# Performance work log

Hardware: AMD Instinct MI355X
Metric: run time of the kernel (lower is better)

## Reference

```python
import jax, jax.numpy as jnp
import numpy as np
from jax import lax

S, T, B, I, H = 10, 256, 128, 128, 128


def setup_inputs() -> dict:
    key = jax.random.key(0)
    ks = jax.random.split(key, 32)
    stdv = 1.0 / np.sqrt(H)
    u = lambda k, shp: jax.random.uniform(k, shp, jnp.float32, -stdv, stdv)
    inp = {
        'features': jax.random.normal(ks[0], (S, T, B, I), jnp.float32),
        # 10 parallel cuDNN-style LSTMs (PyTorch gate order i,f,g,o)
        'lstm_Wih': u(ks[1], (S, 4 * H, I)),
        'lstm_Whh': u(ks[2], (S, 4 * H, H)),
        'lstm_bih': u(ks[3], (S, 4 * H)),
        'lstm_bhh': u(ks[4], (S, 4 * H)),
        # MI-LSTM: per-stream input gate + candidate, shared f/o gates, attention Wa
        'mi_Wi': u(ks[5], (S, H, H)), 'mi_Ui': u(ks[6], (S, H, H)), 'mi_bi': u(ks[7], (S, H)),
        'mi_Wc': u(ks[8], (S, H, H)), 'mi_Uc': u(ks[9], (S, H, H)), 'mi_bc': u(ks[10], (S, H)),
        'mi_Wf': u(ks[11], (H, H)), 'mi_Uf': u(ks[12], (H, H)), 'mi_bf': u(ks[13], (H,)),
        'mi_Wo': u(ks[14], (H, H)), 'mi_Uo': u(ks[15], (H, H)), 'mi_bo': u(ks[16], (H,)),
        'mi_Wa': u(ks[17], (H, H)),
        'head_W': u(ks[18], (H, 1)), 'head_b': u(ks[19], (1,)),
    }
    return inp


def _lstm(x, Wih, Whh, bih, bhh):
    # x: [T,B,I]; returns hidden sequence [T,B,H]
    gx = jnp.einsum('tbi,gi->tbg', x, Wih) + bih + bhh  # [T,B,4H]

    def step(carry, gx_t):
        h, c = carry
        g = gx_t + h @ Whh.T
        i, f, gg, o = jnp.split(g, 4, axis=-1)
        c = jax.nn.sigmoid(f) * c + jax.nn.sigmoid(i) * jnp.tanh(gg)
        h = jax.nn.sigmoid(o) * jnp.tanh(c)
        return (h, c), h

    z = jnp.zeros((x.shape[1], Whh.shape[1]), x.dtype)
    _, hs = lax.scan(step, (z, z), gx)
    return hs


def _forward(features, lstm_Wih, lstm_Whh, lstm_bih, lstm_bhh,
             mi_Wi, mi_Ui, mi_bi, mi_Wc, mi_Uc, mi_bc,
             mi_Wf, mi_Uf, mi_bf, mi_Wo, mi_Uo, mi_bo,
             mi_Wa, head_W, head_b):
    # 10 parallel LSTM streams, relu'd outputs -> [S,T,B,H]
    tilde = jax.nn.relu(jax.vmap(_lstm)(features, lstm_Wih, lstm_Whh, lstm_bih, lstm_bhh))

    # precompute input-side gate projections (time-parallel)
    xi = jnp.einsum('ktbh,khd->tkbd', tilde, mi_Wi) + mi_bi[:, None, :]   # [T,S,B,H]
    xc = jnp.einsum('ktbh,khd->tkbd', tilde, mi_Wc) + mi_bc[:, None, :]
    y = tilde[0]                                                          # mainstream [T,B,H]
    xf = y @ mi_Wf + mi_bf                                                # [T,B,H]
    xo = y @ mi_Wo + mi_bo

    def step(carry, xs):
        h, c = carry
        xi_t, xc_t, xf_t, xo_t = xs
        i = jax.nn.sigmoid(xi_t + jnp.einsum('bh,khd->kbd', h, mi_Ui))    # [S,B,H]
        ctil = jnp.tanh(xc_t + jnp.einsum('bh,khd->kbd', h, mi_Uc))
        l = i * ctil                                                      # per-stream cell update
        # attention over the S streams, keyed on previous cell state
        u = jnp.tanh(jnp.einsum('kbh,bh->kb', l, c @ mi_Wa))              # [S,B]
        alpha = jax.nn.softmax(u, axis=0)
        lmix = jnp.einsum('kb,kbh->bh', alpha, l)                         # [B,H]
        f = jax.nn.sigmoid(xf_t + h @ mi_Uf)
        o = jax.nn.sigmoid(xo_t + h @ mi_Uo)
        c_new = f * c + lmix
        h_new = o * jnp.tanh(c_new)
        return (h_new, c_new), h_new

    z = jnp.zeros((B, H), features.dtype)
    _, hs = lax.scan(step, (z, z), (xi, xc, xf, xo))                      # hs: [T,B,H]

    out = jax.nn.relu(jax.nn.relu(hs) @ head_W + head_b)                  # [T,B,1]
    return out


def reference(features, lstm_Wih, lstm_Whh, lstm_bih, lstm_bhh,
              mi_Wi, mi_Ui, mi_bi, mi_Wc, mi_Uc, mi_bc,
              mi_Wf, mi_Uf, mi_bf, mi_Wo, mi_Uo, mi_bo,
              mi_Wa, head_W, head_b):
    return _forward(features, lstm_Wih, lstm_Whh, lstm_bih, lstm_bhh,
                    mi_Wi, mi_Ui, mi_bi, mi_Wc, mi_Uc, mi_bc,
                    mi_Wf, mi_Uf, mi_bf, mi_Wo, mi_Uo, mi_bo,
                    mi_Wa, head_W, head_b)
```

## Files before the change

kernel.cpp:

```cpp
#include <hip/hip_runtime.h>
#include <math.h>

#define SS 10
#define TT 256
#define BB 128
#define HH 128
#define II 128
#define G4 512
#define ZK 256
#define NCOL 2944
#define NBLK 184

#define SZ_W2T   (SS*ZK*G4)
#define SZ_BIAS2 (SS*G4)
#define SZ_UBIG  (HH*NCOL)
#define SZ_TILDE (SS*TT*BB*HH)
#define SZ_X     (TT*SS*BB*HH)
#define SZ_XFO   (TT*BB*HH)

#define OFF_W2T   0
#define OFF_BIAS2 (OFF_W2T + SZ_W2T)
#define OFF_UBIG  (OFF_BIAS2 + SZ_BIAS2)
#define OFF_TILDE (OFF_UBIG + SZ_UBIG)
#define OFF_XI    (OFF_TILDE + SZ_TILDE)
#define OFF_XC    (OFF_XI + SZ_X)
#define OFF_XF    (OFF_XC + SZ_X)
#define OFF_XO    (OFF_XF + SZ_XFO)
#define OFF_HT    (OFF_XO + SZ_XFO)
#define OFF_CT    (OFF_HT + BB*HH)
#define OFF_ACT   (OFF_CT + BB*HH)
#define OFF_CNT   (OFF_ACT + BB*NCOL)

__device__ __forceinline__ float sigf(float x){ return 1.0f/(1.0f+expf(-x)); }

__device__ __forceinline__ float ald(const float* p){
  return __hip_atomic_load(p, __ATOMIC_RELAXED, __HIP_MEMORY_SCOPE_AGENT);
}
__device__ __forceinline__ void ast(float* p, float v){
  __hip_atomic_store(p, v, __ATOMIC_RELAXED, __HIP_MEMORY_SCOPE_AGENT);
}
__device__ __forceinline__ int aldi(const int* p){
  return __hip_atomic_load(p, __ATOMIC_RELAXED, __HIP_MEMORY_SCOPE_AGENT);
}
__device__ __forceinline__ void asti(int* p, int v){
  __hip_atomic_store(p, v, __ATOMIC_RELAXED, __HIP_MEMORY_SCOPE_AGENT);
}
typedef float f32x4v __attribute__((ext_vector_type(4)));
__device__ __forceinline__ void ast4(float* p, float a, float b, float c, float d){
  f32x4v w; w.x = a; w.y = b; w.z = c; w.w = d;
  asm volatile("global_store_dwordx4 %0, %1, off sc0 sc1" :: "v"(p), "v"(w) : "memory");
}
__device__ __forceinline__ f32x4v ald4(const float* p){
  f32x4v r;
  asm volatile("global_load_dwordx4 %0, %1, off sc0 sc1" : "=v"(r) : "v"(p) : "memory");
  return r;
}

__global__ __launch_bounds__(256) void prep_w2t(const float* __restrict__ Wih, const float* __restrict__ Whh,
                                                const float* __restrict__ bih, const float* __restrict__ bhh,
                                                float* __restrict__ w2t, float* __restrict__ bias2){
  int idx = blockIdx.x*256 + threadIdx.x;
  if (idx < SZ_W2T){
    int q = idx & 3; int j = (idx >> 2) & 511; int kk4 = (idx >> 11) & 63; int s = idx >> 17;
    int kk = kk4*4 + q;
    float v = (kk < II) ? Wih[(s*G4 + j)*II + kk] : Whh[(s*G4 + j)*HH + (kk - II)];
    w2t[idx] = v;
  }
  if (idx < SZ_BIAS2) bias2[idx] = bih[idx] + bhh[idx];
}

__global__ __launch_bounds__(256) void prep_ubig(const float* __restrict__ Ui, const float* __restrict__ Uc,
                                                 const float* __restrict__ Uf, const float* __restrict__ Uo,
                                                 const float* __restrict__ Wa, float* __restrict__ ubig){
  int idx = blockIdx.x*256 + threadIdx.x;
  if (idx >= SZ_UBIG) return;
  int col = idx % NCOL; int h = idx / NCOL;
  float v;
  if (col < 1280){ int k = col >> 7, d = col & 127; v = Ui[(k*HH + h)*HH + d]; }
  else if (col < 2560){ int c2 = col - 1280; int k = c2 >> 7, d = c2 & 127; v = Uc[(k*HH + h)*HH + d]; }
  else if (col < 2688){ v = Uf[h*HH + (col - 2560)]; }
  else if (col < 2816){ v = Uo[h*HH + (col - 2688)]; }
  else               { v = Wa[h*HH + (col - 2816)]; }
  ubig[idx] = v;
}

__global__ __launch_bounds__(256) void init_state(int* flags, float* hR, float* cR){
  int idx = blockIdx.x*256 + threadIdx.x;
  if (idx < 384) flags[idx] = 0;
  if (idx < BB*HH){ hR[idx] = 0.f; cR[idx] = 0.f; }
}

__global__ __launch_bounds__(1024) void lstm_scan(const float* __restrict__ feat, const float* __restrict__ w2t,
                                                  const float* __restrict__ bias2, float* __restrict__ tilde){
  int p = blockIdx.x;
  int g = (p & 7) * 20 + (p >> 3);
  int s = g >> 4; int rb = g & 15; int b0 = rb * 8;
  const int tid = threadIdx.x;
  const int j = tid & 511;
  const int half = tid >> 9;
  __shared__ float z[8][ZK];
  __shared__ float glp[8][G4];
  __shared__ float gl[8][G4];
  const float* w2ts = w2t + (size_t)s*ZK*G4;
  const float* wb = w2ts + ((size_t)(half*32)*G4 + j)*4;
  float bj = (half == 0) ? bias2[s*G4 + j] : 0.f;
  const int r8 = tid >> 7;
  const int k8 = tid & 127;
  float c = 0.f;
  z[r8][128 + k8] = 0.f;
  z[r8][k8] = feat[((s*TT + 0)*BB + (b0 + r8))*II + k8];
  __syncthreads();
  for (int t = 0; t < TT; ++t){
    float acc[8];
    #pragma unroll
    for (int r=0;r<8;++r) acc[r] = bj;
    const float* wp = wb;
    const int kb0 = half*128;
    for (int kk4 = 0; kk4 < 32; ++kk4){
      float4 wv = *(const float4*)wp;
      wp += 4*G4;
      #pragma unroll
      for (int r=0;r<8;++r){
        float4 zv = *(const float4*)&z[r][kb0 + kk4*4];
        acc[r] = fmaf(zv.w, wv.w, fmaf(zv.z, wv.z, fmaf(zv.y, wv.y, fmaf(zv.x, wv.x, acc[r]))));
      }
    }
    if (half == 1){
      #pragma unroll
      for (int r=0;r<8;++r) glp[r][j] = acc[r];
    }
    __syncthreads();
    if (half == 0){
      int gtype = j >> 7;
      #pragma unroll
      for (int r=0;r<8;++r){
        float v = acc[r] + glp[r][j];
        v = (gtype == 2) ? tanhf(v) : sigf(v);
        gl[r][j] = v;
      }
    }
    __syncthreads();
    {
      float si = gl[r8][k8];
      float sf = gl[r8][128 + k8];
      float tg = gl[r8][256 + k8];
      float so = gl[r8][384 + k8];
      c = sf*c + si*tg;
      float h = so*tanhf(c);
      z[r8][128 + k8] = h;
      tilde[((s*TT + t)*BB + (b0 + r8))*HH + k8] = fmaxf(h, 0.f);
      if (t+1 < TT)
        z[r8][k8] = feat[((s*TT + (t+1))*BB + (b0 + r8))*II + k8];
    }
    __syncthreads();
  }
}

__global__ __launch_bounds__(256) void proj_ic(const float* __restrict__ tilde,
                                               const float* __restrict__ Wi, const float* __restrict__ bi,
                                               const float* __restrict__ Wc, const float* __restrict__ bc,
                                               float* __restrict__ xi, float* __restrict__ xc){
  const int k = blockIdx.y;
  const int isc = blockIdx.z;
  const float* W = (isc ? Wc : Wi) + k*HH*HH;
  const float* bias = (isc ? bc : bi) + k*HH;
  float* out = isc ? xc : xi;
  const int m0 = blockIdx.x * 128;
  const int tid = threadIdx.x;
  __shared__ float Wl[HH*HH];
  __shared__ float Al[32*HH];
  for (int u = 0; u < 64; ++u) Wl[u*256 + tid] = W[u*256 + tid];
  const int tx = tid & 31, ty = tid >> 5;
  const int d0 = tx*4;
  float4 bv = *(const float4*)&bias[d0];
  __syncthreads();
  for (int ch = 0; ch < 4; ++ch){
    const float* Arow = tilde + (size_t)(k*TT*BB + m0 + ch*32)*HH;
    #pragma unroll
    for (int u = 0; u < 4; ++u)
      *(float4*)&Al[u*1024 + tid*4] = *(const float4*)&Arow[u*1024 + tid*4];
    __syncthreads();
    float4 a0 = bv, a1 = bv, a2 = bv, a3 = bv;
    for (int h = 0; h < HH; ++h){
      float4 w4 = *(const float4*)&Wl[h*HH + d0];
      float A0 = Al[(ty   )*HH + h], A1 = Al[(ty+ 8)*HH + h];
      float A2 = Al[(ty+16)*HH + h], A3 = Al[(ty+24)*HH + h];
      a0.x = fmaf(A0,w4.x,a0.x); a0.y = fmaf(A0,w4.y,a0.y); a0.z = fmaf(A0,w4.z,a0.z); a0.w = fmaf(A0,w4.w,a0.w);
      a1.x = fmaf(A1,w4.x,a1.x); a1.y = fmaf(A1,w4.y,a1.y); a1.z = fmaf(A1,w4.z,a1.z); a1.w = fmaf(A1,w4.w,a1.w);
      a2.x = fmaf(A2,w4.x,a2.x); a2.y = fmaf(A2,w4.y,a2.y); a2.z = fmaf(A2,w4.z,a2.z); a2.w = fmaf(A2,w4.w,a2.w);
      a3.x = fmaf(A3,w4.x,a3.x); a3.y = fmaf(A3,w4.y,a3.y); a3.z = fmaf(A3,w4.z,a3.z); a3.w = fmaf(A3,w4.w,a3.w);
    }
    float4 accs[4] = {a0,a1,a2,a3};
    #pragma unroll
    for (int i = 0; i < 4; ++i){
      int m = m0 + ch*32 + ty + 8*i;
      int t = m >> 7, b = m & 127;
      *(float4*)&out[((t*SS + k)*BB + b)*HH + d0] = accs[i];
    }
    __syncthreads();
  }
}

__global__ __launch_bounds__(256) void proj_fo(const float* __restrict__ tilde,
                                               const float* __restrict__ Wf, const float* __restrict__ bf,
                                               const float* __restrict__ Wo, const float* __restrict__ bo,
                                               float* __restrict__ xf, float* __restrict__ xo){
  const int iso = blockIdx.y;
  const float* W = iso ? Wo : Wf;
  const float* bias = iso ? bo : bf;
  float* out = iso ? xo : xf;
  const int m0 = blockIdx.x * 128;
  const int tid = threadIdx.x;
  __shared__ float Wl[HH*HH];
  __shared__ float Al[32*HH];
  for (int u = 0; u < 64; ++u) Wl[u*256 + tid] = W[u*256 + tid];
  const int tx = tid & 31, ty = tid >> 5;
  const int d0 = tx*4;
  float4 bv = *(const float4*)&bias[d0];
  __syncthreads();
  for (int ch = 0; ch < 4; ++ch){
    const float* Arow = tilde + (size_t)(m0 + ch*32)*HH;
    #pragma unroll
    for (int u = 0; u < 4; ++u)
      *(float4*)&Al[u*1024 + tid*4] = *(const float4*)&Arow[u*1024 + tid*4];
    __syncthreads();
    float4 a0 = bv, a1 = bv, a2 = bv, a3 = bv;
    for (int h = 0; h < HH; ++h){
      float4 w4 = *(const float4*)&Wl[h*HH + d0];
      float A0 = Al[(ty   )*HH + h], A1 = Al[(ty+ 8)*HH + h];
      float A2 = Al[(ty+16)*HH + h], A3 = Al[(ty+24)*HH + h];
      a0.x = fmaf(A0,w4.x,a0.x); a0.y = fmaf(A0,w4.y,a0.y); a0.z = fmaf(A0,w4.z,a0.z); a0.w = fmaf(A0,w4.w,a0.w);
      a1.x = fmaf(A1,w4.x,a1.x); a1.y = fmaf(A1,w4.y,a1.y); a1.z = fmaf(A1,w4.z,a1.z); a1.w = fmaf(A1,w4.w,a1.w);
      a2.x = fmaf(A2,w4.x,a2.x); a2.y = fmaf(A2,w4.y,a2.y); a2.z = fmaf(A2,w4.z,a2.z); a2.w = fmaf(A2,w4.w,a2.w);
      a3.x = fmaf(A3,w4.x,a3.x); a3.y = fmaf(A3,w4.y,a3.y); a3.z = fmaf(A3,w4.z,a3.z); a3.w = fmaf(A3,w4.w,a3.w);
    }
    float4 accs[4] = {a0,a1,a2,a3};
    #pragma unroll
    for (int i = 0; i < 4; ++i){
      int m = m0 + ch*32 + ty + 8*i;
      *(float4*)&out[(size_t)m*HH + d0] = accs[i];
    }
    __syncthreads();
  }
}

__global__ __launch_bounds__(512) void mi_coop(
    const float* __restrict__ ubig,
    const float* __restrict__ xi, const float* __restrict__ xc,
    const float* __restrict__ xf, const float* __restrict__ xo,
    const float* __restrict__ headW, const float* __restrict__ headb,
    float* hR, float* cR,
    float* act, int* flags, float* __restrict__ out)
{
  const int bk = blockIdx.x;
  const int tid = threadIdx.x;
  __shared__ float Wl[128*132];
  __shared__ __align__(16) float hLT[128*20];
  __shared__ __align__(16) float pan[4*2564];
  __shared__ float lL[10*128];
  __shared__ float part[8][8];
  __shared__ float uL[10];

  const int rg = bk / 23, cg = bk - rg*23;
  const int rb0 = rg*16;
  int btype; int xk = 0;
  if (cg < 10){ btype = 0; xk = cg; }
  else if (cg < 20){ btype = 1; xk = cg - 10; }
  else if (cg == 20) btype = 2;
  else if (cg == 21) btype = 3;
  else btype = 4;

  for (int idx = tid; idx < 128*128; idx += 512){
    int h = idx >> 7, c = idx & 127;
    Wl[h*132 + (c ^ (((h>>5)&1)<<2))] = ubig[(size_t)h*NCOL + cg*128 + c];
  }

  const int dsl = tid & 3, ctl = (tid >> 2) & 15, rt = tid >> 6;
  const int c0g = ctl*8;
  const int pkey = (ctl & 3) << 2;

  const int erow = tid >> 5, ec0 = (tid & 31) * 4;
  const float* xrd = nullptr; size_t xrd_step = 0;
  if (btype == 0){ xrd = xi + ((size_t)xk*BB + rb0 + erow)*HH + ec0; xrd_step = (size_t)SS*BB*HH; }
  else if (btype == 1){ xrd = xc + ((size_t)xk*BB + rb0 + erow)*HH + ec0; xrd_step = (size_t)SS*BB*HH; }
  else if (btype == 2){ xrd = xf + (size_t)(rb0 + erow)*HH + ec0; xrd_step = (size_t)BB*HH; }
  else if (btype == 3){ xrd = xo + (size_t)(rb0 + erow)*HH + ec0; xrd_step = (size_t)BB*HH; }

  const bool isP = (bk < BB);
  const int pb = bk;
  const int rgP = pb >> 4;
  const int wv = tid >> 6, lane = tid & 63;
  float c_reg = 0.f;
  float hw = headW[tid & 127];
  float hb = headb[0];

  int* flag_g = flags;
  int* flag_p = flags + 192;
  const float* arow = act + (size_t)pb*NCOL;

  for (int t = 0; t < TT; ++t){
    float4 xv = make_float4(0.f, 0.f, 0.f, 0.f);
    if (btype != 4) xv = *(const float4*)(xrd + (size_t)t*xrd_step);
    if (tid < 16){
      while (aldi(&flag_p[rb0 + tid]) < t) __builtin_amdgcn_s_sleep(1);
    }
    __syncthreads();
    asm volatile("" ::: "memory");
    const float* src = (btype == 4) ? cR : hR;
    {
      int bl = tid >> 5;
      int d4 = (tid & 31) * 4;
      f32x4v sv = ald4(&src[(size_t)(rb0 + bl)*HH + d4]);
      asm volatile("s_waitcnt vmcnt(0)" ::: "memory");
      int slot = bl ^ (((d4 >> 4) & 3) << 2);
      hLT[(d4+0)*20 + slot] = sv.x;
      hLT[(d4+1)*20 + slot] = sv.y;
      hLT[(d4+2)*20 + slot] = sv.z;
      hLT[(d4+3)*20 + slot] = sv.w;
    }
    __syncthreads();
    if (tid < 128){
      float acc[8][8];
      #pragma unroll
      for (int i = 0; i < 8; ++i)
        #pragma unroll
        for (int j = 0; j < 8; ++j) acc[i][j] = 0.f;
      const int wkey = (dsl & 1) << 2;
      #pragma unroll 4
      for (int dd = 0; dd < 32; ++dd){
        int d = dsl*32 + dd;
        int akey = ((d >> 4) & 3) << 2;
        float4 a0 = *(const float4*)&hLT[d*20 + ((rt*8)     ^ akey)];
        float4 a1 = *(const float4*)&hLT[d*20 + ((rt*8 + 4) ^ akey)];
        float4 w0 = *(const float4*)&Wl[d*132 + ((c0g)      ^ wkey)];
        float4 w1 = *(const float4*)&Wl[d*132 + ((c0g + 4)  ^ wkey)];
        float a[8] = {a0.x, a0.y, a0.z, a0.w, a1.x, a1.y, a1.z, a1.w};
        float w[8] = {w0.x, w0.y, w0.z, w0.w, w1.x, w1.y, w1.z, w1.w};
        #pragma unroll
        for (int i = 0; i < 8; ++i)
          #pragma unroll
          for (int j = 0; j < 8; ++j)
            acc[i][j] = fmaf(a[i], w[j], acc[i][j]);
      }
      float* pt = pan + dsl*2564;
      #pragma unroll
      for (int j = 0; j < 8; ++j){
        int cb = (c0g + j)*20;
        *(float4*)&pt[cb + ((rt*8)     ^ pkey)] = make_float4(acc[0][j], acc[1][j], acc[2][j], acc[3][j]);
        *(float4*)&pt[cb + ((rt*8 + 4) ^ pkey)] = make_float4(acc[4][j], acc[5][j], acc[6][j], acc[7][j]);
      }
    }
    __syncthreads();
    {
      float xvals[4] = {xv.x, xv.y, xv.z, xv.w};
      float vout[4];
      #pragma unroll
      for (int u = 0; u < 4; ++u){
        int col = ec0 + u;
        int slot = erow ^ (((col >> 3) & 3) << 2);
        int cb = col*20 + slot;
        float pv = pan[cb] + pan[2564 + cb] + pan[2*2564 + cb] + pan[3*2564 + cb] + xvals[u];
        float v;
        if (btype == 1) v = tanhf(pv);
        else if (btype == 4) v = pv;
        else v = sigf(pv);
        vout[u] = v;
      }
      float* ap = &act[(size_t)(rb0 + erow)*NCOL + (size_t)cg*128 + ec0];
      ast4(ap, vout[0], vout[1], vout[2], vout[3]);
    }
    asm volatile("s_waitcnt vmcnt(0)" ::: "memory");
    __syncthreads();
    if (tid == 0) asti(&flag_g[bk], t + 1);
    if (isP && tid < 23){
      while (aldi(&flag_g[rgP*23 + tid]) < t + 1) __builtin_amdgcn_s_sleep(1);
    }
    __syncthreads();
    asm volatile("" ::: "memory");
    if (isP){
      float cw0 = ald(&arow[2816 + lane]);
      float cw1 = ald(&arow[2816 + lane + 64]);
      #pragma unroll
      for (int kk2 = 0; kk2 < 2; ++kk2){
        if (kk2 == 0 || wv < 2){
          int k = wv + kk2*8;
          float li0 = ald(&arow[k*128 + lane])      * ald(&arow[1280 + k*128 + lane]);
          float li1 = ald(&arow[k*128 + lane + 64]) * ald(&arow[1280 + k*128 + lane + 64]);
          lL[k*128 + lane] = li0;
          lL[k*128 + lane + 64] = li1;
          float s = li0*cw0 + li1*cw1;
          s += __shfl_down(s, 32); s += __shfl_down(s, 16); s += __shfl_down(s, 8);
          s += __shfl_down(s, 4);  s += __shfl_down(s, 2);  s += __shfl_down(s, 1);
          if (lane == 0) uL[k] = tanhf(s);
        }
      }
    }
    __syncthreads();
    if (isP && tid < 128){
      float m = uL[0];
      #pragma unroll
      for (int k = 1; k < 10; ++k) m = fmaxf(m, uL[k]);
      float e[10]; float es = 0.f;
      #pragma unroll
      for (int k = 0; k < 10; ++k){ e[k] = expf(uL[k] - m); es += e[k]; }
      float inv = 1.f / es;
      float lm = 0.f;
      #pragma unroll
      for (int k = 0; k < 10; ++k) lm = fmaf(e[k]*inv, lL[k*128 + tid], lm);
      float f = ald(&arow[2560 + tid]);
      float o = ald(&arow[2688 + tid]);
      float cn = fmaf(f, c_reg, lm);
      float hn = o * tanhf(cn);
      c_reg = cn;
      ast(&hR[pb*HH + tid], hn);
      ast(&cR[pb*HH + tid], cn);
      float s = fmaxf(hn, 0.f) * hw;
      s += __shfl_down(s, 32); s += __shfl_down(s, 16); s += __shfl_down(s, 8);
      s += __shfl_down(s, 4);  s += __shfl_down(s, 2);  s += __shfl_down(s, 1);
      if ((tid & 63) == 0) part[wv][6] = s;
    }
    __syncthreads();
    if (isP && tid == 0)
      out[t*BB + pb] = fmaxf(part[0][6] + part[1][6] + hb, 0.f);
    asm volatile("s_waitcnt vmcnt(0)" ::: "memory");
    __syncthreads();
    if (isP && tid == 0) asti(&flag_p[pb], t + 1);
  }
}

extern "C" void kernel_launch(void* const* d_in, const int* in_sizes, int n_in,
                              void* d_out, int out_size, void* d_ws, size_t ws_size,
                              hipStream_t stream) {
  const float* feat  = (const float*)d_in[0];
  const float* Wih   = (const float*)d_in[1];
  const float* Whh   = (const float*)d_in[2];
  const float* bih   = (const float*)d_in[3];
  const float* bhh   = (const float*)d_in[4];
  const float* miWi  = (const float*)d_in[5];
  const float* miUi  = (const float*)d_in[6];
  const float* mibi  = (const float*)d_in[7];
  const float* miWc  = (const float*)d_in[8];
  const float* miUc  = (const float*)d_in[9];
  const float* mibc  = (const float*)d_in[10];
  const float* miWf  = (const float*)d_in[11];
  const float* miUf  = (const float*)d_in[12];
  const float* mibf  = (const float*)d_in[13];
  const float* miWo  = (const float*)d_in[14];
  const float* miUo  = (const float*)d_in[15];
  const float* mibo  = (const float*)d_in[16];
  const float* miWa  = (const float*)d_in[17];
  const float* headW = (const float*)d_in[18];
  const float* headb = (const float*)d_in[19];
  float* out = (float*)d_out;

  float* ws    = (float*)d_ws;
  float* w2t   = ws + OFF_W2T;
  float* bias2 = ws + OFF_BIAS2;
  float* ubig  = ws + OFF_UBIG;
  float* tilde = ws + OFF_TILDE;
  float* xi    = ws + OFF_XI;
  float* xc    = ws + OFF_XC;
  float* xf    = ws + OFF_XF;
  float* xo    = ws + OFF_XO;
  float* hR    = ws + OFF_HT;
  float* cR    = ws + OFF_CT;
  float* act   = ws + OFF_ACT;
  int*   flags = (int*)(ws + OFF_CNT);

  prep_w2t<<<dim3(SZ_W2T/256), dim3(256), 0, stream>>>(Wih, Whh, bih, bhh, w2t, bias2);
  prep_ubig<<<dim3((SZ_UBIG+255)/256), dim3(256), 0, stream>>>(miUi, miUc, miUf, miUo, miWa, ubig);
  init_state<<<dim3(64), dim3(256), 0, stream>>>(flags, hR, cR);
  lstm_scan<<<dim3(160), dim3(1024), 0, stream>>>(feat, w2t, bias2, tilde);
  proj_ic<<<dim3(256, SS, 2), dim3(256), 0, stream>>>(tilde, miWi, mibi, miWc, mibc, xi, xc);
  proj_fo<<<dim3(256, 2), dim3(256), 0, stream>>>(tilde, miWf, mibf, miWo, mibo, xf, xo);

  void* kargs[] = { (void*)&ubig, (void*)&xi, (void*)&xc, (void*)&xf, (void*)&xo,
                    (void*)&headW, (void*)&headb, (void*)&hR, (void*)&cR,
                    (void*)&act, (void*)&flags, (void*)&out };
  hipLaunchCooperativeKernel((const void*)mi_coop, dim3(NBLK), dim3(512), kargs, 0, stream);
}
```

Before: 6.784 ms.

## Remove LSTM gate sync stage and spread MI-LSTM matvec over more threads

In the stream LSTM scan kernel, both halves now write their partial gate sums to shared memory and the cell-update threads add them, apply the bias and compute the activations directly. This drops one barrier and the separate activation pass per timestep, and the inner k loop is now unrolled. In the cooperative MI-LSTM kernel, the recurrent matvec is split across 256 threads with 8x4 tiles instead of 128 threads with 8x8, using new padded and swizzled shared-memory layouts to avoid bank conflicts. This targets per-step latency on the serial recurrence, at the cost of more shared-memory traffic and more complex indexing.

```diff
diff --git a/kernel.cpp b/kernel.cpp
--- a/kernel.cpp
+++ b/kernel.cpp
@@ -99,13 +99,15 @@
   const int j = tid & 511;
   const int half = tid >> 9;
   __shared__ float z[8][ZK];
-  __shared__ float glp[8][G4];
-  __shared__ float gl[8][G4];
+  __shared__ float glp[2][8][G4];
   const float* w2ts = w2t + (size_t)s*ZK*G4;
   const float* wb = w2ts + ((size_t)(half*32)*G4 + j)*4;
-  float bj = (half == 0) ? bias2[s*G4 + j] : 0.f;
   const int r8 = tid >> 7;
   const int k8 = tid & 127;
+  float b_i = bias2[s*G4 + k8];
+  float b_f = bias2[s*G4 + 128 + k8];
+  float b_g = bias2[s*G4 + 256 + k8];
+  float b_o = bias2[s*G4 + 384 + k8];
   float c = 0.f;
   z[r8][128 + k8] = 0.f;
   z[r8][k8] = feat[((s*TT + 0)*BB + (b0 + r8))*II + k8];
@@ -113,9 +115,10 @@
   for (int t = 0; t < TT; ++t){
     float acc[8];
     #pragma unroll
-    for (int r=0;r<8;++r) acc[r] = bj;
+    for (int r=0;r<8;++r) acc[r] = 0.f;
     const float* wp = wb;
     const int kb0 = half*128;
+    #pragma unroll 4
     for (int kk4 = 0; kk4 < 32; ++kk4){
       float4 wv = *(const float4*)wp;
       wp += 4*G4;
@@ -125,28 +128,17 @@
         acc[r] = fmaf(zv.w, wv.w, fmaf(zv.z, wv.z, fmaf(zv.y, wv.y, fmaf(zv.x, wv.x, acc[r]))));
       }
     }
-    if (half == 1){
-      #pragma unroll
-      for (int r=0;r<8;++r) glp[r][j] = acc[r];
-    }
-    __syncthreads();
-    if (half == 0){
-      int gtype = j >> 7;
-      #pragma unroll
-      for (int r=0;r<8;++r){
-        float v = acc[r] + glp[r][j];
-        v = (gtype == 2) ? tanhf(v) : sigf(v);
-        gl[r][j] = v;
-      }
-    }
+    #pragma unroll
+    for (int r=0;r<8;++r) glp[half][r][j] = acc[r];
     __syncthreads();
     {
-      float si = gl[r8][k8];
-      float sf = gl[r8][128 + k8];
-      float tg = gl[r8][256 + k8];
-      float so = gl[r8][384 + k8];
-      c = sf*c + si*tg;
-      float h = so*tanhf(c);
+      float gi = glp[0][r8][k8]       + glp[1][r8][k8]       + b_i;
+      float gf = glp[0][r8][128 + k8] + glp[1][r8][128 + k8] + b_f;
+      float gg = glp[0][r8][256 + k8] + glp[1][r8][256 + k8] + b_g;
+      float go = glp[0][r8][384 + k8] + glp[1][r8][384 + k8] + b_o;
+      float i_ = sigf(gi), f_ = sigf(gf), g_ = tanhf(gg), o_ = sigf(go);
+      c = f_*c + i_*g_;
+      float h = o_*tanhf(c);
       z[r8][128 + k8] = h;
       tilde[((s*TT + t)*BB + (b0 + r8))*HH + k8] = fmaxf(h, 0.f);
       if (t+1 < TT)
@@ -254,9 +246,9 @@
 {
   const int bk = blockIdx.x;
   const int tid = threadIdx.x;
-  __shared__ float Wl[128*132];
-  __shared__ __align__(16) float hLT[128*20];
-  __shared__ __align__(16) float pan[4*2564];
+  __shared__ float Wl[16928];
+  __shared__ __align__(16) float hLT[2584];
+  __shared__ __align__(16) float pan[4*2584];
   __shared__ float lL[10*128];
   __shared__ float part[8][8];
   __shared__ float uL[10];
@@ -272,12 +264,13 @@
 
   for (int idx = tid; idx < 128*128; idx += 512){
     int h = idx >> 7, c = idx & 127;
-    Wl[h*132 + (c ^ (((h>>5)&1)<<2))] = ubig[(size_t)h*NCOL + cg*128 + c];
-  }
-
-  const int dsl = tid & 3, ctl = (tid >> 2) & 15, rt = tid >> 6;
-  const int c0g = ctl*8;
-  const int pkey = (ctl & 3) << 2;
+    Wl[h*132 + ((h>>5)<<3) + (c ^ (((c>>3)&3)<<2))] = ubig[(size_t)h*NCOL + cg*128 + c];
+  }
+
+  const int dsl = tid & 3, ctl2 = (tid >> 2) & 31, rt = (tid >> 7) & 1;
+  const int c0g = ctl2*4;
+  const int keyc = ((ctl2 >> 1) & 3) << 2;
+  const int pkey2 = (ctl2 & 3) << 2;
 
   const int erow = tid >> 5, ec0 = (tid & 31) * 4;
   const float* xrd = nullptr; size_t xrd_step = 0;
@@ -312,42 +305,43 @@
       int d4 = (tid & 31) * 4;
       f32x4v sv = ald4(&src[(size_t)(rb0 + bl)*HH + d4]);
       asm volatile("s_waitcnt vmcnt(0)" ::: "memory");
+      int base = d4*20 + ((d4>>5)<<3);
       int slot = bl ^ (((d4 >> 4) & 3) << 2);
-      hLT[(d4+0)*20 + slot] = sv.x;
-      hLT[(d4+1)*20 + slot] = sv.y;
-      hLT[(d4+2)*20 + slot] = sv.z;
-      hLT[(d4+3)*20 + slot] = sv.w;
-    }
-    __syncthreads();
-    if (tid < 128){
-      float acc[8][8];
+      hLT[base + slot]      = sv.x;
+      hLT[base + 20 + slot] = sv.y;
+      hLT[base + 40 + slot] = sv.z;
+      hLT[base + 60 + slot] = sv.w;
+    }
+    __syncthreads();
+    if (tid < 256){
+      float acc[8][4];
       #pragma unroll
       for (int i = 0; i < 8; ++i)
         #pragma unroll
-        for (int j = 0; j < 8; ++j) acc[i][j] = 0.f;
-      const int wkey = (dsl & 1) << 2;
+        for (int j = 0; j < 4; ++j) acc[i][j] = 0.f;
       #pragma unroll 4
       for (int dd = 0; dd < 32; ++dd){
-        int d = dsl*32 + dd;
+        int d = (dsl << 5) + dd;
         int akey = ((d >> 4) & 3) << 2;
-        float4 a0 = *(const float4*)&hLT[d*20 + ((rt*8)     ^ akey)];
-        float4 a1 = *(const float4*)&hLT[d*20 + ((rt*8 + 4) ^ akey)];
-        float4 w0 = *(const float4*)&Wl[d*132 + ((c0g)      ^ wkey)];
-        float4 w1 = *(const float4*)&Wl[d*132 + ((c0g + 4)  ^ wkey)];
+        int hb2 = d*20 + (dsl << 3);
+        float4 a0 = *(const float4*)&hLT[hb2 + ((rt*8)     ^ akey)];
+        float4 a1 = *(const float4*)&hLT[hb2 + ((rt*8 + 4) ^ akey)];
+        float4 w4 = *(const float4*)&Wl[d*132 + (dsl << 3) + (c0g ^ keyc)];
         float a[8] = {a0.x, a0.y, a0.z, a0.w, a1.x, a1.y, a1.z, a1.w};
-        float w[8] = {w0.x, w0.y, w0.z, w0.w, w1.x, w1.y, w1.z, w1.w};
+        float w[4] = {w4.x, w4.y, w4.z, w4.w};
         #pragma unroll
         for (int i = 0; i < 8; ++i)
           #pragma unroll
-          for (int j = 0; j < 8; ++j)
+          for (int j = 0; j < 4; ++j)
             acc[i][j] = fmaf(a[i], w[j], acc[i][j]);
       }
-      float* pt = pan + dsl*2564;
-      #pragma unroll
-      for (int j = 0; j < 8; ++j){
-        int cb = (c0g + j)*20;
-        *(float4*)&pt[cb + ((rt*8)     ^ pkey)] = make_float4(acc[0][j], acc[1][j], acc[2][j], acc[3][j]);
-        *(float4*)&pt[cb + ((rt*8 + 4) ^ pkey)] = make_float4(acc[4][j], acc[5][j], acc[6][j], acc[7][j]);
+      float* pt = pan + dsl*2584;
+      #pragma unroll
+      for (int j = 0; j < 4; ++j){
+        int col = c0g + j;
+        int cb = col*20 + ((col>>5)<<3);
+        *(float4*)&pt[cb + ((rt*8)     ^ pkey2)] = make_float4(acc[0][j], acc[1][j], acc[2][j], acc[3][j]);
+        *(float4*)&pt[cb + ((rt*8 + 4) ^ pkey2)] = make_float4(acc[4][j], acc[5][j], acc[6][j], acc[7][j]);
       }
     }
     __syncthreads();
@@ -357,9 +351,9 @@
       #pragma unroll
       for (int u = 0; u < 4; ++u){
         int col = ec0 + u;
-        int slot = erow ^ (((col >> 3) & 3) << 2);
-        int cb = col*20 + slot;
-        float pv = pan[cb] + pan[2564 + cb] + pan[2*2564 + cb] + pan[3*2564 + cb] + xvals[u];
+        int slot = erow ^ (((col >> 2) & 3) << 2);
+        int cb = col*20 + ((col>>5)<<3) + slot;
+        float pv = pan[cb] + pan[2584 + cb] + pan[2*2584 + cb] + pan[3*2584 + cb] + xvals[u];
         float v;
         if (btype == 1) v = tanhf(pv);
         else if (btype == 4) v = pv;
```

Result: faster. 6.338 ms (-6.6%).
